# Optimization experiments

Hardware: AMD Instinct MI355X
Metric: run time of the kernel (lower is better)

## Reference

```python
import jax, jax.numpy as jnp
import numpy as np

B, K, N, T, C = 2, 2, 4096, 8, 3
H = 192            # hidden_dim
NODE_DIM = 10
N_LAYERS = 10
KNN = 16           # k nearest neighbours
TOP_FRAC = 0.4
SHARP = 5.0        # mask_sharpness
S = max(int(TOP_FRAC * N), KNN + 1)   # n_select per graph


def _ln(x, g, b, eps=1e-5):
    mu = x.mean(-1, keepdims=True)
    v = ((x - mu) ** 2).mean(-1, keepdims=True)  # biased var, matches nn.LayerNorm
    return (x - mu) / jnp.sqrt(v + eps) * g + b


def setup_inputs() -> dict:
    key = jax.random.key(0)
    ks = jax.random.split(key, 12)
    rn = lambda k, shape: 0.05 * jax.random.normal(k, shape, jnp.float32)
    F0 = 2 * NODE_DIM + 4   # first EdgeConv MLP in-dim
    FR = 2 * H + 4          # remaining EdgeConv MLP in-dim
    L = N_LAYERS - 1
    return {
        "u_base": jax.random.normal(ks[0], (B, K, N, C), jnp.float32),
        "pos": jax.random.uniform(ks[1], (B, N, 3), dtype=jnp.float32),
        "velocity_in": jax.random.normal(ks[2], (B, T, N, C), jnp.float32),
        "airfoil_mask": (jax.random.uniform(ks[3], (B, N)) < 0.05).astype(jnp.float32),
        "conv0_w1": rn(ks[4], (F0, H)), "conv0_b1": jnp.zeros((H,)),
        "conv0_w2": rn(ks[5], (H, H)), "conv0_b2": jnp.zeros((H,)),
        "conv0_g": jnp.ones((H,)), "conv0_be": jnp.zeros((H,)),
        "convs_w1": rn(ks[6], (L, FR, H)), "convs_b1": jnp.zeros((L, H)),
        "convs_w2": rn(ks[7], (L, H, H)), "convs_b2": jnp.zeros((L, H)),
        "convs_g": jnp.ones((L, H)), "convs_be": jnp.zeros((L, H)),
        "head_g": jnp.ones((H,)), "head_be": jnp.zeros((H,)),
        "head_w1": rn(ks[8], (H, H)), "head_b1": jnp.zeros((H,)),
        "head_w2": rn(ks[9], (H, 3)), "head_b2": jnp.zeros((3,)),
    }


def reference(u_base, pos, velocity_in, airfoil_mask,
              conv0_w1, conv0_b1, conv0_w2, conv0_b2, conv0_g, conv0_be,
              convs_w1, convs_b1, convs_w2, convs_b2, convs_g, convs_be,
              head_g, head_be, head_w1, head_b1, head_w2, head_b2):
    # --- variance gating (torch .var/.std are unbiased) ---
    var_pp = jnp.var(velocity_in, axis=1, ddof=1).sum(-1)                      # [B,N]
    var_z = (var_pp - var_pp.mean(1, keepdims=True)) / (
        jnp.std(var_pp, axis=1, ddof=1, keepdims=True) + 1e-8)
    soft_mask = jax.nn.sigmoid(SHARP * var_z) * (1.0 - airfoil_mask)           # [B,N]

    # --- select top-variance points per graph ---
    _, top_idx = jax.lax.top_k(var_pp, S)                                      # [B,S]
    pos_sel = jnp.take_along_axis(pos, top_idx[..., None], axis=1)             # [B,S,3]
    mask_sel = jnp.take_along_axis(soft_mask, top_idx, axis=1)[..., None]      # [B,S,1]
    v_last = velocity_in[:, -1]                                                # [B,N,C]
    ub_sel = jnp.take_along_axis(u_base, top_idx[:, None, :, None], axis=2)    # [B,K,S,C]
    vl_sel = jnp.take_along_axis(v_last, top_idx[..., None], axis=1)           # [B,S,C]
    vf_sel = jnp.take_along_axis(var_pp[..., None], top_idx[..., None], axis=1)
    static = jnp.concatenate([vl_sel, pos_sel, vf_sel], -1)                    # [B,S,7]
    x0 = jnp.concatenate(
        [ub_sel, jnp.broadcast_to(static[:, None], (B, K, S, 7))], -1)         # [B,K,S,10]

    def per_graph(x, pos_b):  # x: [K,S,F0], pos_b: [S,3]
        # kNN graph (self excluded via +inf diagonal, as in the chunked cdist)
        d2 = jnp.sum((pos_b[:, None] - pos_b[None]) ** 2, -1)                  # [S,S]
        d2 = d2.at[jnp.arange(S), jnp.arange(S)].set(jnp.inf)
        _, knn = jax.lax.top_k(-d2, KNN)                                       # [S,KNN]
        # PyG convention with edge_index=stack([targets, sources]):
        # i = edge_index[1] = knn neighbours, j = edge_index[0] = centre nodes
        idx_i = knn.reshape(-1)                     # [E] aggregation targets
        idx_j = jnp.repeat(jnp.arange(S), KNN)      # [E]
        rel = pos_b[idx_i] - pos_b[idx_j]           # pos[edge_index[1]] - pos[edge_index[0]]
        dist = jnp.linalg.norm(rel, axis=-1, keepdims=True)
        ea = jnp.concatenate([rel, dist], -1)       # [E,4]
        ea_b = jnp.broadcast_to(ea, (K,) + ea.shape)

        def conv(h, w1, b1, w2, b2, g, be):
            hi = h[:, idx_i]
            hj = h[:, idx_j]
            m = jnp.concatenate([hi, hj - hi, ea_b], -1)                       # [K,E,2F+4]
            m = jax.nn.gelu(m @ w1 + b1, approximate=False) @ w2 + b2          # [K,E,H]
            agg = jnp.zeros((K, S, H), h.dtype).at[:, idx_i].add(m)
            return _ln(agg, g, be)

        h = conv(x, conv0_w1, conv0_b1, conv0_w2, conv0_b2, conv0_g, conv0_be)
        for l in range(N_LAYERS - 1):
            h = conv(h, convs_w1[l], convs_b1[l], convs_w2[l], convs_b2[l],
                     convs_g[l], convs_be[l]) + h
        hh = _ln(h, head_g, head_be)
        return jax.nn.gelu(hh @ head_w1 + head_b1, approximate=False) @ head_w2 + head_b2

    delta = jax.vmap(per_graph)(x0, pos_sel)        # [B,K,S,3]
    delta = delta * mask_sel[:, None]               # [B,1,S,1]

    def scatter_b(idx, d):  # idx [S], d [K,S,3]
        return jnp.zeros((K, N, C), d.dtype).at[:, idx].set(d)

    delta_full = jax.vmap(scatter_b)(top_idx, delta)            # [B,K,N,C]
    return (u_base + delta_full) * (1.0 - airfoil_mask)[:, None, :, None]
```

## Files before the change

kernel.cpp:

```cpp
#include <hip/hip_runtime.h>
#include <hip/hip_bf16.h>
#include <math.h>

#define B_ 2
#define K_ 2
#define NN_ 4096
#define T_ 8
#define C_ 3
#define H_ 192
#define S_ 1638
#define KK_ 16
#define E_ (S_*KK_)
#define NROW (B_*K_*S_)
#define SHARP_ 5.0f

typedef __hip_bfloat16 bf;
typedef unsigned long long ull;
typedef __bf16 bf16x8 __attribute__((ext_vector_type(8)));
typedef float f32x4 __attribute__((ext_vector_type(4)));

__device__ int   g_isbf16;
__device__ int   g_viol;
__device__ __align__(16) float g_var[B_*NN_];
__device__ __align__(16) float g_soft[B_*NN_];
__device__ __align__(16) float g_accum[B_*2];
__device__ __align__(16) int   g_topidx[B_*S_];
__device__ __align__(16) float g_possel[B_*S_*3];
__device__ __align__(16) float g_masksel[B_*S_];
__device__ __align__(16) float g_x0[NROW*10];
__device__ __align__(16) int   g_knn[B_*E_];
__device__ __align__(16) float g_ea[B_*E_*4];
__device__ __align__(16) int   g_indeg[B_*S_];
__device__ __align__(16) int   g_cursor[B_*S_];
__device__ __align__(16) int   g_off[B_*(S_+1)];
__device__ __align__(16) int   g_list[B_*E_];
__device__ __align__(16) float g_P[(size_t)NROW*H_];
__device__ __align__(16) bf    g_Qbf[(size_t)NROW*H_];
__device__ __align__(16) float g_h[(size_t)NROW*H_];
__device__ __align__(16) bf    g_hbf[(size_t)NROW*H_];
__device__ __align__(16) bf    g_abf[(size_t)NROW*H_];
__device__ __align__(16) bf    g_hh[(size_t)NROW*H_];
__device__ __align__(16) bf    g_t[(size_t)NROW*H_];
__device__ __align__(16) bf    g_w2p[(size_t)11*H_*H_];
__device__ __align__(16) bf    g_wcp[(size_t)9*H_*384];

__device__ __forceinline__ float bf2f(bf x){ return __bfloat162float(x); }
__device__ __forceinline__ float LD(const void* p, long i){
  return g_isbf16 ? __bfloat162float(((const bf*)p)[i]) : ((const float*)p)[i];
}
__device__ __forceinline__ float gelu_f(float x){ return 0.5f*x*(1.0f + erff(x*0.70710678118654752f)); }
__device__ __forceinline__ ull shfl_xor_u64(ull v, int m){
  unsigned lo = (unsigned)v, hi = (unsigned)(v >> 32);
  lo = __shfl_xor(lo, m, 64); hi = __shfl_xor(hi, m, 64);
  return ((ull)hi << 32) | lo;
}

__global__ void k_viol(const void* a, const void* b, const void* c){
  int t = threadIdx.x;
  const bf* pa = (const bf*)a; const bf* pb = (const bf*)b; const bf* pc = (const bf*)c;
  int bad = 0;
  #pragma unroll
  for (int s = 0; s < 2; ++s){
    float va = __bfloat162float(pa[t + s*256]);
    float vb = __bfloat162float(pb[t + s*256]);
    float vc = __bfloat162float(pc[t + s*256]);
    if (!(fabsf(va) <= 1000.f)) bad = 1;
    if (!(fabsf(vb) <= 1000.f)) bad = 1;
    if (!(fabsf(vc) <= 1000.f)) bad = 1;
  }
  if (threadIdx.x == 0) g_viol = 0;
  __syncthreads();
  if (bad) atomicOr(&g_viol, 1);
  __syncthreads();
  if (threadIdx.x == 0) g_isbf16 = (g_viol == 0) ? 1 : 0;
}

__global__ void k_zero(){
  int tid = blockIdx.x*256 + threadIdx.x;
  if (tid < B_*S_){ g_indeg[tid]=0; g_cursor[tid]=0; }
  if (tid < B_*2) g_accum[tid]=0.f;
}

__global__ void k_var(const void* __restrict__ vel){
  int b = blockIdx.y;
  int n = blockIdx.x*256 + threadIdx.x;
  float v = 0.f;
  #pragma unroll
  for (int c = 0; c < 3; ++c){
    float x[8];
    #pragma unroll
    for (int t = 0; t < 8; ++t)
      x[t] = LD(vel, ((long)(b*T_+t)*NN_ + n)*3 + c);
    float m = __fadd_rn(__fadd_rn(__fadd_rn(x[0],x[1]), __fadd_rn(x[2],x[3])),
                        __fadd_rn(__fadd_rn(x[4],x[5]), __fadd_rn(x[6],x[7]))) / 8.0f;
    float d[8];
    #pragma unroll
    for (int t = 0; t < 8; ++t){ float dd = __fadd_rn(x[t], -m); d[t] = __fmul_rn(dd,dd); }
    float sv = __fadd_rn(__fadd_rn(__fadd_rn(d[0],d[1]), __fadd_rn(d[2],d[3])),
                         __fadd_rn(__fadd_rn(d[4],d[5]), __fadd_rn(d[6],d[7])));
    v = __fadd_rn(v, sv / 7.0f);
  }
  g_var[b*NN_ + n] = v;
  float s1 = v, s2 = v*v;
  #pragma unroll
  for (int o = 32; o; o >>= 1){ s1 += __shfl_xor(s1,o,64); s2 += __shfl_xor(s2,o,64); }
  __shared__ float r1[4], r2[4];
  int lane = threadIdx.x & 63, wid = threadIdx.x >> 6;
  if (!lane){ r1[wid]=s1; r2[wid]=s2; }
  __syncthreads();
  if (threadIdx.x == 0){
    atomicAdd(&g_accum[b*2+0], r1[0]+r1[1]+r1[2]+r1[3]);
    atomicAdd(&g_accum[b*2+1], r2[0]+r2[1]+r2[2]+r2[3]);
  }
}

__global__ void k_soft(const void* __restrict__ air){
  int b = blockIdx.y;
  int n = blockIdx.x*256 + threadIdx.x;
  float S1 = g_accum[b*2], S2 = g_accum[b*2+1];
  float mean = S1*(1.f/NN_);
  float sd = sqrtf(fmaxf((S2 - S1*S1*(1.f/NN_))*(1.f/(NN_-1)), 0.f));
  float v = g_var[b*NN_+n];
  float z = (v-mean)/(sd+1e-8f);
  float sig = 1.f/(1.f+expf(-SHARP_*z));
  g_soft[b*NN_+n] = sig*(1.f - LD(air, b*NN_+n));
}

__global__ __launch_bounds__(256) void k_rank(){
  int b = blockIdx.y;
  int i = blockIdx.x*4 + (threadIdx.x >> 6);
  int lane = threadIdx.x & 63;
  float vi = g_var[b*NN_+i];
  int rank = 0;
  for (int j = lane; j < NN_; j += 64){
    float vj = g_var[b*NN_+j];
    rank += ((vj > vi) || (vj == vi && j < i)) ? 1 : 0;
  }
  #pragma unroll
  for (int o = 32; o; o >>= 1) rank += __shfl_xor(rank, o, 64);
  if (lane == 0 && rank < S_) g_topidx[b*S_ + rank] = i;
}

__global__ void k_gather(const void* __restrict__ pos, const void* __restrict__ ub,
                         const void* __restrict__ vel){
  int gi = blockIdx.x*256 + threadIdx.x;
  if (gi >= B_*S_) return;
  int b = gi / S_, s = gi - b*S_;
  int node = g_topidx[gi];
  float px = LD(pos, ((long)b*NN_+node)*3+0);
  float py = LD(pos, ((long)b*NN_+node)*3+1);
  float pz = LD(pos, ((long)b*NN_+node)*3+2);
  g_possel[gi*3+0]=px; g_possel[gi*3+1]=py; g_possel[gi*3+2]=pz;
  g_masksel[gi] = g_soft[b*NN_+node];
  float vf = g_var[b*NN_+node];
  float vl0 = LD(vel, ((long)(b*T_+7)*NN_+node)*3+0);
  float vl1 = LD(vel, ((long)(b*T_+7)*NN_+node)*3+1);
  float vl2 = LD(vel, ((long)(b*T_+7)*NN_+node)*3+2);
  for (int k = 0; k < K_; ++k){
    long row = (long)(b*K_+k)*S_ + s;
    float* x = g_x0 + row*10;
    x[0]=LD(ub, ((long)(b*K_+k)*NN_+node)*3+0);
    x[1]=LD(ub, ((long)(b*K_+k)*NN_+node)*3+1);
    x[2]=LD(ub, ((long)(b*K_+k)*NN_+node)*3+2);
    x[3]=vl0; x[4]=vl1; x[5]=vl2;
    x[6]=px;  x[7]=py;  x[8]=pz;
    x[9]=vf;
  }
}

__global__ __launch_bounds__(256) void k_knn(){
  __shared__ float px[S_], py[S_], pz[S_];
  int b = blockIdx.y;
  int j = blockIdx.x*4 + (threadIdx.x >> 6);
  int lane = threadIdx.x & 63;
  for (int t = threadIdx.x; t < S_; t += 256){
    px[t] = g_possel[(b*S_+t)*3+0];
    py[t] = g_possel[(b*S_+t)*3+1];
    pz[t] = g_possel[(b*S_+t)*3+2];
  }
  __syncthreads();
  if (j >= S_) return;
  float xj=px[j], yj=py[j], zj=pz[j];
  float dist[KK_]; int id[KK_];
  #pragma unroll
  for (int t = 0; t < KK_; ++t){ dist[t]=3.0e38f; id[t]=0x7fffffff; }
  for (int c = lane; c < S_; c += 64){
    if (c == j) continue;
    float dx=__fadd_rn(px[c],-xj), dy=__fadd_rn(py[c],-yj), dz=__fadd_rn(pz[c],-zj);
    float d2 = __fadd_rn(__fadd_rn(__fmul_rn(dx,dx), __fmul_rn(dy,dy)), __fmul_rn(dz,dz));
    if (d2 < dist[KK_-1]){
      int p = 0;
      #pragma unroll
      for (int q = 0; q < KK_; ++q) p += (dist[q] <= d2) ? 1 : 0;
      #pragma unroll
      for (int q = KK_-1; q >= 1; --q){
        bool mv = (q > p);
        dist[q] = mv ? dist[q-1] : dist[q];
        id[q]   = mv ? id[q-1]   : id[q];
      }
      #pragma unroll
      for (int q = 0; q < KK_; ++q){ if (q == p){ dist[q] = d2; id[q] = c; } }
    }
  }
  ull mykey = 0;
  #pragma unroll
  for (int t = 0; t < KK_; ++t){
    ull k = (((ull)__float_as_uint(dist[0])) << 32) | (unsigned)id[0];
    ull m = k;
    #pragma unroll
    for (int o = 32; o; o >>= 1){ ull other = shfl_xor_u64(m, o); m = (other < m) ? other : m; }
    if (k == m){
      #pragma unroll
      for (int q = 0; q < KK_-1; ++q){ dist[q]=dist[q+1]; id[q]=id[q+1]; }
      dist[KK_-1] = 3.0e38f; id[KK_-1] = 0x7fffffff;
    }
    if (lane == t) mykey = m;
  }
  if (lane < KK_){
    int i = (int)(mykey & 0xffffffffu);
    g_knn[(b*S_+j)*KK_ + lane] = i;
    float rx = __fadd_rn(px[i],-xj), ry = __fadd_rn(py[i],-yj), rz = __fadd_rn(pz[i],-zj);
    float dd = sqrtf(__fadd_rn(__fadd_rn(__fmul_rn(rx,rx), __fmul_rn(ry,ry)), __fmul_rn(rz,rz)));
    float* o = g_ea + ((long)b*E_ + j*KK_ + lane)*4;
    o[0]=rx; o[1]=ry; o[2]=rz; o[3]=dd;
    atomicAdd(&g_indeg[b*S_+i], 1);
  }
}

__global__ void k_scan(){
  __shared__ int sA[2048], sB[2048];
  int b = blockIdx.x, tid = threadIdx.x;
  for (int i = tid; i < 2048; i += 1024) sA[i] = (i < S_) ? g_indeg[b*S_+i] : 0;
  __syncthreads();
  int *src = sA, *dst = sB;
  for (int d = 1; d < 2048; d <<= 1){
    for (int i = tid; i < 2048; i += 1024) dst[i] = src[i] + (i >= d ? src[i-d] : 0);
    __syncthreads();
    int* t2 = src; src = dst; dst = t2;
  }
  if (tid == 0) g_off[b*(S_+1)] = 0;
  for (int i = tid; i < S_; i += 1024) g_off[b*(S_+1)+i+1] = src[i];
}

__global__ void k_fill(){
  int idx = blockIdx.x*256 + threadIdx.x;
  if (idx >= B_*E_) return;
  int b = idx / E_, e = idx - b*E_;
  int i = g_knn[idx];
  int slot = atomicAdd(&g_cursor[b*S_+i], 1);
  g_list[b*E_ + g_off[b*(S_+1)+i] + slot] = e;
}

__global__ void k_pack_w2(const void* __restrict__ c0w2, const void* __restrict__ cw2,
                          const void* __restrict__ hw1){
  int gi = blockIdx.x*256 + threadIdx.x;
  if (gi >= 11*H_*H_) return;
  int mat = gi / (H_*H_), r = gi - mat*(H_*H_);
  int k = r / H_, n = r - (r/H_)*H_;
  float v;
  if (mat == 0)      v = LD(c0w2, (long)k*H_ + n);
  else if (mat <= 9) v = LD(cw2, (long)(mat-1)*H_*H_ + (long)k*H_ + n);
  else               v = LD(hw1, (long)k*H_ + n);
  int t = k>>5, q = (k>>3)&3, jj = k&7;
  g_w2p[(size_t)mat*H_*H_ + (((t*4+q)*H_ + n)*8 + jj)] = __float2bfloat16(v);
}

__global__ void k_pack_wc(const void* __restrict__ cw1){
  int gi = blockIdx.x*256 + threadIdx.x;
  if (gi >= 9*H_*384) return;
  int l = gi / (H_*384), r = gi - l*(H_*384);
  int k = r / 384, n = r - (r/384)*384;
  long base = (long)l*388*H_;
  float v;
  if (n < H_) v = LD(cw1, base + (long)k*H_ + n) - LD(cw1, base + (long)(H_+k)*H_ + n);
  else        v = LD(cw1, base + (long)(H_+k)*H_ + (n-H_));
  int t = k>>5, q = (k>>3)&3, jj = k&7;
  g_wcp[(size_t)l*(H_*384) + (((t*4+q)*384 + n)*8 + jj)] = __float2bfloat16(v);
}

__global__ void k_proj0(const void* __restrict__ w1){
  int gi = blockIdx.x*256 + threadIdx.x;
  if (gi >= NROW*384) return;
  int row = gi / 384, n = gi - (gi/384)*384;
  const float* x = g_x0 + (size_t)row*10;
  float acc = 0.f;
  if (n < H_){
    #pragma unroll
    for (int f = 0; f < 10; ++f) acc += x[f] * (LD(w1, f*H_+n) - LD(w1, (10+f)*H_+n));
    g_P[(size_t)row*H_ + n] = acc;
  } else {
    int hc = n - H_;
    #pragma unroll
    for (int f = 0; f < 10; ++f) acc += x[f] * LD(w1, (10+f)*H_+hc);
    g_Qbf[(size_t)row*H_ + hc] = __float2bfloat16(acc);
  }
}

__global__ __launch_bounds__(256) void k_gemmPQ(int bOff, int M){
  const bf* A  = g_hbf;
  const bf* Bp = g_wcp + bOff;
  int wave = threadIdx.x >> 6, lane = threadIdx.x & 63;
  int q = lane >> 4, l16 = lane & 15;
  long rowBase = (long)blockIdx.x * 32;
  f32x4 acc[2][6];
  #pragma unroll
  for (int rt = 0; rt < 2; ++rt)
    #pragma unroll
    for (int ct = 0; ct < 6; ++ct) acc[rt][ct] = (f32x4){0.f,0.f,0.f,0.f};
  #pragma unroll
  for (int t = 0; t < 6; ++t){
    int kof = t*32 + q*8;
    bf16x8 af[2], bfr[6];
    #pragma unroll
    for (int rt = 0; rt < 2; ++rt){
      long r = rowBase + rt*16 + l16;
      if (r >= M) r = M-1;
      af[rt] = *reinterpret_cast<const bf16x8*>(A + r*192 + kof);
    }
    #pragma unroll
    for (int ct = 0; ct < 6; ++ct){
      int n = wave*96 + ct*16 + l16;
      bfr[ct] = *reinterpret_cast<const bf16x8*>(Bp + (((t*4+q)*384 + n)*8));
    }
    #pragma unroll
    for (int rt = 0; rt < 2; ++rt)
      #pragma unroll
      for (int ct = 0; ct < 6; ++ct)
        acc[rt][ct] = __builtin_amdgcn_mfma_f32_16x16x32_bf16(af[rt], bfr[ct], acc[rt][ct], 0,0,0);
  }
  #pragma unroll
  for (int rt = 0; rt < 2; ++rt){
    #pragma unroll
    for (int ct = 0; ct < 6; ++ct){
      int col = wave*96 + ct*16 + l16;
      #pragma unroll
      for (int r = 0; r < 4; ++r){
        long row = rowBase + rt*16 + q*4 + r;
        if (row < M){
          float v = acc[rt][ct][r];
          if (col < 192) g_P[row*192 + col] = v;
          else           g_Qbf[row*192 + (col-192)] = __float2bfloat16(v);
        }
      }
    }
  }
}

template<int RES>
__global__ __launch_bounds__(256) void k_gemmln(const void* __restrict__ biasB, long biasO,
                                                const void* __restrict__ gB, long gO,
                                                const void* __restrict__ beB, long beO,
                                                int bOff, int M){
  const bf* A  = g_abf;
  const bf* Bp = g_w2p + bOff;
  int wave = threadIdx.x >> 6, lane = threadIdx.x & 63;
  int q = lane >> 4, l16 = lane & 15;
  long rowBase = (long)blockIdx.x * 32;
  f32x4 acc[2][3];
  #pragma unroll
  for (int rt = 0; rt < 2; ++rt)
    #pragma unroll
    for (int ct = 0; ct < 3; ++ct) acc[rt][ct] = (f32x4){0.f,0.f,0.f,0.f};
  #pragma unroll
  for (int t = 0; t < 6; ++t){
    int kof = t*32 + q*8;
    bf16x8 af[2], bfr[3];
    #pragma unroll
    for (int rt = 0; rt < 2; ++rt){
      long r = rowBase + rt*16 + l16;
      if (r >= M) r = M-1;
      af[rt] = *reinterpret_cast<const bf16x8*>(A + r*192 + kof);
    }
    #pragma unroll
    for (int ct = 0; ct < 3; ++ct){
      int n = wave*48 + ct*16 + l16;
      bfr[ct] = *reinterpret_cast<const bf16x8*>(Bp + (((t*4+q)*192 + n)*8));
    }
    #pragma unroll
    for (int rt = 0; rt < 2; ++rt)
      #pragma unroll
      for (int ct = 0; ct < 3; ++ct)
        acc[rt][ct] = __builtin_amdgcn_mfma_f32_16x16x32_bf16(af[rt], bfr[ct], acc[rt][ct], 0,0,0);
  }
  __shared__ float tile[32][200];
  __shared__ float srow[32], rrow[32];
  #pragma unroll
  for (int rt = 0; rt < 2; ++rt){
    #pragma unroll
    for (int ct = 0; ct < 3; ++ct){
      int col = wave*48 + ct*16 + l16;
      float bb = LD(biasB, biasO + col);
      #pragma unroll
      for (int r = 0; r < 4; ++r){
        int lr = rt*16 + q*4 + r;
        long row = rowBase + lr;
        long rowc = (row < M) ? row : (M-1);
        int bk = (int)(rowc / S_); int i = (int)(rowc - (long)bk*S_); int b = bk >> 1;
        float degf = (float)(g_off[b*(S_+1)+i+1] - g_off[b*(S_+1)+i]);
        tile[lr][col] = acc[rt][ct][r] + degf*bb;
      }
    }
  }
  __syncthreads();
  {
    int lr = threadIdx.x >> 3;
    int k8 = threadIdx.x & 7;
    float s = 0.f, qq = 0.f;
    for (int c = k8; c < 192; c += 8){ float x = tile[lr][c]; s += x; qq += x*x; }
    #pragma unroll
    for (int o = 1; o < 8; o <<= 1){ s += __shfl_xor(s,o,64); qq += __shfl_xor(qq,o,64); }
    if (k8 == 0){
      float mu = s*(1.f/H_);
      float var = qq*(1.f/H_) - mu*mu;
      srow[lr] = mu;
      rrow[lr] = rsqrtf(fmaxf(var, 0.f) + 1e-5f);
    }
  }
  __syncthreads();
  #pragma unroll
  for (int rt = 0; rt < 2; ++rt){
    #pragma unroll
    for (int ct = 0; ct < 3; ++ct){
      int col = wave*48 + ct*16 + l16;
      float gg = LD(gB, gO+col), be = LD(beB, beO+col);
      #pragma unroll
      for (int r = 0; r < 4; ++r){
        int lr = rt*16 + q*4 + r;
        long row = rowBase + lr;
        if (row < M){
          float y = (tile[lr][col] - srow[lr])*rrow[lr]*gg + be;
          if (RES) y += g_h[row*192 + col];
          g_h[row*192 + col] = y;
          g_hbf[row*192 + col] = __float2bfloat16(y);
        }
      }
    }
  }
}

__global__ __launch_bounds__(256) void k_gemmhead(const void* __restrict__ biasB,
                                                  int bOff, int M){
  const bf* A  = g_hh;
  const bf* Bp = g_w2p + bOff;
  int wave = threadIdx.x >> 6, lane = threadIdx.x & 63;
  int q = lane >> 4, l16 = lane & 15;
  long rowBase = (long)blockIdx.x * 32;
  f32x4 acc[2][3];
  #pragma unroll
  for (int rt = 0; rt < 2; ++rt)
    #pragma unroll
    for (int ct = 0; ct < 3; ++ct) acc[rt][ct] = (f32x4){0.f,0.f,0.f,0.f};
  #pragma unroll
  for (int t = 0; t < 6; ++t){
    int kof = t*32 + q*8;
    bf16x8 af[2], bfr[3];
    #pragma unroll
    for (int rt = 0; rt < 2; ++rt){
      long r = rowBase + rt*16 + l16;
      if (r >= M) r = M-1;
      af[rt] = *reinterpret_cast<const bf16x8*>(A + r*192 + kof);
    }
    #pragma unroll
    for (int ct = 0; ct < 3; ++ct){
      int n = wave*48 + ct*16 + l16;
      bfr[ct] = *reinterpret_cast<const bf16x8*>(Bp + (((t*4+q)*192 + n)*8));
    }
    #pragma unroll
    for (int rt = 0; rt < 2; ++rt)
      #pragma unroll
      for (int ct = 0; ct < 3; ++ct)
        acc[rt][ct] = __builtin_amdgcn_mfma_f32_16x16x32_bf16(af[rt], bfr[ct], acc[rt][ct], 0,0,0);
  }
  #pragma unroll
  for (int rt = 0; rt < 2; ++rt){
    #pragma unroll
    for (int ct = 0; ct < 3; ++ct){
      int col = wave*48 + ct*16 + l16;
      float bb = LD(biasB, col);
      #pragma unroll
      for (int r = 0; r < 4; ++r){
        long row = rowBase + rt*16 + q*4 + r;
        if (row < M) g_t[row*192 + col] = __float2bfloat16(gelu_f(acc[rt][ct][r] + bb));
      }
    }
  }
}

__global__ __launch_bounds__(192) void k_aggedge(const void* __restrict__ w1cB, long w1cO,
                                                 const void* __restrict__ b1B, long b1O){
  int row = blockIdx.x;
  int col = threadIdx.x;
  int bk = row / S_, i = row - bk*S_, b = bk >> 1;
  int off = g_off[b*(S_+1)+i];
  int deg = g_off[b*(S_+1)+i+1] - off;
  float w0 = LD(w1cB, w1cO+col),       w1v = LD(w1cB, w1cO+H_+col);
  float w2v = LD(w1cB, w1cO+2*H_+col), w3v = LD(w1cB, w1cO+3*H_+col);
  float base = g_P[(size_t)row*H_ + col] + LD(b1B, b1O+col);
  const int* lst = g_list + b*E_ + off;
  const bf* Q = g_Qbf + (size_t)bk*S_*H_;
  const float* EA = g_ea + (size_t)b*E_*4;
  float acc = 0.f;
  int d = 0;
  for (; d + 4 <= deg; d += 4){
    int e0 = lst[d], e1 = lst[d+1], e2 = lst[d+2], e3 = lst[d+3];
    float4 a0 = *reinterpret_cast<const float4*>(EA + (size_t)e0*4);
    float4 a1 = *reinterpret_cast<const float4*>(EA + (size_t)e1*4);
    float4 a2 = *reinterpret_cast<const float4*>(EA + (size_t)e2*4);
    float4 a3 = *reinterpret_cast<const float4*>(EA + (size_t)e3*4);
    float q0 = bf2f(Q[(size_t)(e0>>4)*H_ + col]);
    float q1 = bf2f(Q[(size_t)(e1>>4)*H_ + col]);
    float q2 = bf2f(Q[(size_t)(e2>>4)*H_ + col]);
    float q3 = bf2f(Q[(size_t)(e3>>4)*H_ + col]);
    acc += gelu_f(base + q0 + a0.x*w0 + a0.y*w1v + a0.z*w2v + a0.w*w3v);
    acc += gelu_f(base + q1 + a1.x*w0 + a1.y*w1v + a1.z*w2v + a1.w*w3v);
    acc += gelu_f(base + q2 + a2.x*w0 + a2.y*w1v + a2.z*w2v + a2.w*w3v);
    acc += gelu_f(base + q3 + a3.x*w0 + a3.y*w1v + a3.z*w2v + a3.w*w3v);
  }
  for (; d < deg; ++d){
    int e = lst[d];
    float4 a = *reinterpret_cast<const float4*>(EA + (size_t)e*4);
    float qv = bf2f(Q[(size_t)(e>>4)*H_ + col]);
    acc += gelu_f(base + qv + a.x*w0 + a.y*w1v + a.z*w2v + a.w*w3v);
  }
  g_abf[(size_t)row*H_ + col] = __float2bfloat16(acc);
}

__global__ void k_lnhead(const void* __restrict__ g, const void* __restrict__ be){
  int row = blockIdx.x;
  int col = threadIdx.x;
  float x = g_h[(size_t)row*H_ + col];
  float s = x, qq = x*x;
  #pragma unroll
  for (int o = 32; o; o >>= 1){ s += __shfl_xor(s,o,64); qq += __shfl_xor(qq,o,64); }
  __shared__ float ws[3][2];
  int wid = col >> 6, lane = col & 63;
  if (!lane){ ws[wid][0]=s; ws[wid][1]=qq; }
  __syncthreads();
  float Sm = ws[0][0]+ws[1][0]+ws[2][0];
  float Qm = ws[0][1]+ws[1][1]+ws[2][1];
  float mu = Sm*(1.f/H_);
  float var = Qm*(1.f/H_) - mu*mu;
  float rstd = rsqrtf(fmaxf(var, 0.f) + 1e-5f);
  g_hh[(size_t)row*H_ + col] = __float2bfloat16((x-mu)*rstd*LD(g,col) + LD(be,col));
}

__global__ void k_initout(const void* __restrict__ ub, const void* __restrict__ air, float* __restrict__ out){
  int gi = blockIdx.x*256 + threadIdx.x;
  int n = (gi/3) % NN_;
  int b = gi / (K_*NN_*C_);
  float a = 1.f - LD(air, b*NN_+n);
  out[gi] = LD(ub, gi) * a;
}

__global__ void k_headout(const void* __restrict__ w2, const void* __restrict__ b2,
                          const void* __restrict__ ub, const void* __restrict__ air,
                          float* __restrict__ out){
  int row = blockIdx.x*4 + (threadIdx.x >> 6);
  int lane = threadIdx.x & 63;
  if (row >= NROW) return;
  float t0 = bf2f(g_t[(size_t)row*H_ + lane]);
  float t1 = bf2f(g_t[(size_t)row*H_ + lane + 64]);
  float t2 = bf2f(g_t[(size_t)row*H_ + lane + 128]);
  float d[3];
  #pragma unroll
  for (int c = 0; c < 3; ++c){
    float p = t0*LD(w2,lane*3+c) + t1*LD(w2,(lane+64)*3+c) + t2*LD(w2,(lane+128)*3+c);
    #pragma unroll
    for (int o = 32; o; o >>= 1) p += __shfl_xor(p,o,64);
    d[c] = p + LD(b2,c);
  }
  if (lane == 0){
    int bk = row / S_, s = row - bk*S_, b = bk >> 1;
    float msk = g_masksel[b*S_+s];
    int node = g_topidx[b*S_+s];
    float am = 1.f - LD(air, b*NN_+node);
    #pragma unroll
    for (int c = 0; c < 3; ++c){
      long oi = ((long)bk*NN_ + node)*3 + c;
      out[oi] = (LD(ub,oi) + d[c]*msk)*am;
    }
  }
}

extern "C" void kernel_launch(void* const* d_in, const int* in_sizes, int n_in,
                              void* d_out, int out_size, void* d_ws, size_t ws_size,
                              hipStream_t stream) {
  (void)in_sizes; (void)n_in; (void)d_ws; (void)ws_size; (void)out_size;
  const void* u_base = d_in[0];
  const void* pos    = d_in[1];
  const void* vel    = d_in[2];
  const void* air    = d_in[3];
  const void* c0w1   = d_in[4];
  const void* c0b1   = d_in[5];
  const void* c0w2   = d_in[6];
  const void* c0b2   = d_in[7];
  const void* c0g    = d_in[8];
  const void* c0be   = d_in[9];
  const void* cw1    = d_in[10];
  const void* cb1    = d_in[11];
  const void* cw2    = d_in[12];
  const void* cb2    = d_in[13];
  const void* cg     = d_in[14];
  const void* cbe    = d_in[15];
  const void* hg     = d_in[16];
  const void* hbe    = d_in[17];
  const void* hw1    = d_in[18];
  const void* hb1    = d_in[19];
  const void* hw2    = d_in[20];
  const void* hb2    = d_in[21];
  float* out = (float*)d_out;

  k_viol<<<1, 256, 0, stream>>>(u_base, pos, vel);
  k_zero<<<13, 256, 0, stream>>>();
  k_var<<<dim3(16, B_), 256, 0, stream>>>(vel);
  k_soft<<<dim3(16, B_), 256, 0, stream>>>(air);
  k_rank<<<dim3(NN_/4, B_), 256, 0, stream>>>();
  k_gather<<<13, 256, 0, stream>>>(pos, u_base, vel);
  k_knn<<<dim3((S_+3)/4, B_), 256, 0, stream>>>();
  k_scan<<<B_, 1024, 0, stream>>>();
  k_fill<<<205, 256, 0, stream>>>();
  k_pack_w2<<<1584, 256, 0, stream>>>(c0w2, cw2, hw1);
  k_pack_wc<<<2592, 256, 0, stream>>>(cw1);
  k_initout<<<192, 256, 0, stream>>>(u_base, air, out);
  k_proj0<<<9828, 256, 0, stream>>>(c0w1);

  const int GN = (NROW + 31) / 32;
  for (int l = 0; l < 10; ++l){
    if (l > 0) k_gemmPQ<<<GN, 256, 0, stream>>>((l-1)*H_*384, NROW);

    long w1cO = (l == 0) ? 20L*H_ : ((long)(l-1)*388 + 384)*H_;
    const void* w1cB = (l == 0) ? c0w1 : cw1;
    long lOff = (l == 0) ? 0 : (long)(l-1)*H_;
    const void* b1B = (l == 0) ? c0b1 : cb1;
    k_aggedge<<<NROW, 192, 0, stream>>>(w1cB, w1cO, b1B, lOff);

    const void* b2B = (l == 0) ? c0b2 : cb2;
    const void* gB  = (l == 0) ? c0g  : cg;
    const void* beB = (l == 0) ? c0be : cbe;
    if (l > 0) k_gemmln<1><<<GN, 256, 0, stream>>>(b2B, lOff, gB, lOff, beB, lOff, l*H_*H_, NROW);
    else       k_gemmln<0><<<GN, 256, 0, stream>>>(b2B, lOff, gB, lOff, beB, lOff, l*H_*H_, NROW);
  }

  k_lnhead<<<NROW, 192, 0, stream>>>(hg, hbe);
  k_gemmhead<<<GN, 256, 0, stream>>>(hb1, 10*H_*H_, NROW);
  k_headout<<<NROW/4, 256, 0, stream>>>(hw2, hb2, u_base, air, out);
}
```

Measured before the change: 679.5 us.

## Fuse next-layer PQ projection into GEMM+LN epilogue and LN into head GEMM

Each layer's W2 GEMM + LayerNorm kernel now stages the normalized bf16 hidden state in shared memory and immediately runs the next layer's PQ projection GEMM from it. This removes the separate k_gemmPQ launch and the global g_hbf round trip. The head LayerNorm is folded into the head GEMM, and the soft-mask computation is moved into the gather kernel. k_viol/k_zero are merged and proj0 is tiled with weights cached in shared memory. The cost is higher shared memory and register use per block, which may lower occupancy.

```diff
diff --git a/kernel.cpp b/kernel.cpp
--- a/kernel.cpp
+++ b/kernel.cpp
@@ -22,7 +22,6 @@
 __device__ int   g_isbf16;
 __device__ int   g_viol;
 __device__ __align__(16) float g_var[B_*NN_];
-__device__ __align__(16) float g_soft[B_*NN_];
 __device__ __align__(16) float g_accum[B_*2];
 __device__ __align__(16) int   g_topidx[B_*S_];
 __device__ __align__(16) float g_possel[B_*S_*3];
@@ -37,9 +36,7 @@
 __device__ __align__(16) float g_P[(size_t)NROW*H_];
 __device__ __align__(16) bf    g_Qbf[(size_t)NROW*H_];
 __device__ __align__(16) float g_h[(size_t)NROW*H_];
-__device__ __align__(16) bf    g_hbf[(size_t)NROW*H_];
 __device__ __align__(16) bf    g_abf[(size_t)NROW*H_];
-__device__ __align__(16) bf    g_hh[(size_t)NROW*H_];
 __device__ __align__(16) bf    g_t[(size_t)NROW*H_];
 __device__ __align__(16) bf    g_w2p[(size_t)11*H_*H_];
 __device__ __align__(16) bf    g_wcp[(size_t)9*H_*384];
@@ -55,30 +52,29 @@
   return ((ull)hi << 32) | lo;
 }
 
-__global__ void k_viol(const void* a, const void* b, const void* c){
-  int t = threadIdx.x;
-  const bf* pa = (const bf*)a; const bf* pb = (const bf*)b; const bf* pc = (const bf*)c;
-  int bad = 0;
-  #pragma unroll
-  for (int s = 0; s < 2; ++s){
-    float va = __bfloat162float(pa[t + s*256]);
-    float vb = __bfloat162float(pb[t + s*256]);
-    float vc = __bfloat162float(pc[t + s*256]);
-    if (!(fabsf(va) <= 1000.f)) bad = 1;
-    if (!(fabsf(vb) <= 1000.f)) bad = 1;
-    if (!(fabsf(vc) <= 1000.f)) bad = 1;
-  }
-  if (threadIdx.x == 0) g_viol = 0;
-  __syncthreads();
-  if (bad) atomicOr(&g_viol, 1);
-  __syncthreads();
-  if (threadIdx.x == 0) g_isbf16 = (g_viol == 0) ? 1 : 0;
-}
-
-__global__ void k_zero(){
+__global__ void k_vz(const void* a, const void* b, const void* c){
   int tid = blockIdx.x*256 + threadIdx.x;
   if (tid < B_*S_){ g_indeg[tid]=0; g_cursor[tid]=0; }
   if (tid < B_*2) g_accum[tid]=0.f;
+  if (blockIdx.x == 0){
+    int t = threadIdx.x;
+    const bf* pa = (const bf*)a; const bf* pb = (const bf*)b; const bf* pc = (const bf*)c;
+    int bad = 0;
+    #pragma unroll
+    for (int s = 0; s < 2; ++s){
+      float va = __bfloat162float(pa[t + s*256]);
+      float vb = __bfloat162float(pb[t + s*256]);
+      float vc = __bfloat162float(pc[t + s*256]);
+      if (!(fabsf(va) <= 1000.f)) bad = 1;
+      if (!(fabsf(vb) <= 1000.f)) bad = 1;
+      if (!(fabsf(vc) <= 1000.f)) bad = 1;
+    }
+    if (threadIdx.x == 0) g_viol = 0;
+    __syncthreads();
+    if (bad) atomicOr(&g_viol, 1);
+    __syncthreads();
+    if (threadIdx.x == 0) g_isbf16 = (g_viol == 0) ? 1 : 0;
+  }
 }
 
 __global__ void k_var(const void* __restrict__ vel){
@@ -112,18 +108,6 @@
     atomicAdd(&g_accum[b*2+0], r1[0]+r1[1]+r1[2]+r1[3]);
     atomicAdd(&g_accum[b*2+1], r2[0]+r2[1]+r2[2]+r2[3]);
   }
-}
-
-__global__ void k_soft(const void* __restrict__ air){
-  int b = blockIdx.y;
-  int n = blockIdx.x*256 + threadIdx.x;
-  float S1 = g_accum[b*2], S2 = g_accum[b*2+1];
-  float mean = S1*(1.f/NN_);
-  float sd = sqrtf(fmaxf((S2 - S1*S1*(1.f/NN_))*(1.f/(NN_-1)), 0.f));
-  float v = g_var[b*NN_+n];
-  float z = (v-mean)/(sd+1e-8f);
-  float sig = 1.f/(1.f+expf(-SHARP_*z));
-  g_soft[b*NN_+n] = sig*(1.f - LD(air, b*NN_+n));
 }
 
 __global__ __launch_bounds__(256) void k_rank(){
@@ -142,7 +126,7 @@
 }
 
 __global__ void k_gather(const void* __restrict__ pos, const void* __restrict__ ub,
-                         const void* __restrict__ vel){
+                         const void* __restrict__ vel, const void* __restrict__ air){
   int gi = blockIdx.x*256 + threadIdx.x;
   if (gi >= B_*S_) return;
   int b = gi / S_, s = gi - b*S_;
@@ -151,8 +135,13 @@
   float py = LD(pos, ((long)b*NN_+node)*3+1);
   float pz = LD(pos, ((long)b*NN_+node)*3+2);
   g_possel[gi*3+0]=px; g_possel[gi*3+1]=py; g_possel[gi*3+2]=pz;
-  g_masksel[gi] = g_soft[b*NN_+node];
+  float S1 = g_accum[b*2], S2 = g_accum[b*2+1];
+  float mean = S1*(1.f/NN_);
+  float sd = sqrtf(fmaxf((S2 - S1*S1*(1.f/NN_))*(1.f/(NN_-1)), 0.f));
   float vf = g_var[b*NN_+node];
+  float z = (vf-mean)/(sd+1e-8f);
+  float sig = 1.f/(1.f+expf(-SHARP_*z));
+  g_masksel[gi] = sig*(1.f - LD(air, b*NN_+node));
   float vl0 = LD(vel, ((long)(b*T_+7)*NN_+node)*3+0);
   float vl1 = LD(vel, ((long)(b*T_+7)*NN_+node)*3+1);
   float vl2 = LD(vel, ((long)(b*T_+7)*NN_+node)*3+2);
@@ -278,210 +267,37 @@
   g_wcp[(size_t)l*(H_*384) + (((t*4+q)*384 + n)*8 + jj)] = __float2bfloat16(v);
 }
 
-__global__ void k_proj0(const void* __restrict__ w1){
-  int gi = blockIdx.x*256 + threadIdx.x;
-  if (gi >= NROW*384) return;
-  int row = gi / 384, n = gi - (gi/384)*384;
-  const float* x = g_x0 + (size_t)row*10;
-  float acc = 0.f;
-  if (n < H_){
-    #pragma unroll
-    for (int f = 0; f < 10; ++f) acc += x[f] * (LD(w1, f*H_+n) - LD(w1, (10+f)*H_+n));
-    g_P[(size_t)row*H_ + n] = acc;
-  } else {
-    int hc = n - H_;
-    #pragma unroll
-    for (int f = 0; f < 10; ++f) acc += x[f] * LD(w1, (10+f)*H_+hc);
-    g_Qbf[(size_t)row*H_ + hc] = __float2bfloat16(acc);
-  }
-}
-
-__global__ __launch_bounds__(256) void k_gemmPQ(int bOff, int M){
-  const bf* A  = g_hbf;
-  const bf* Bp = g_wcp + bOff;
-  int wave = threadIdx.x >> 6, lane = threadIdx.x & 63;
-  int q = lane >> 4, l16 = lane & 15;
-  long rowBase = (long)blockIdx.x * 32;
-  f32x4 acc[2][6];
-  #pragma unroll
-  for (int rt = 0; rt < 2; ++rt)
-    #pragma unroll
-    for (int ct = 0; ct < 6; ++ct) acc[rt][ct] = (f32x4){0.f,0.f,0.f,0.f};
-  #pragma unroll
-  for (int t = 0; t < 6; ++t){
-    int kof = t*32 + q*8;
-    bf16x8 af[2], bfr[6];
-    #pragma unroll
-    for (int rt = 0; rt < 2; ++rt){
-      long r = rowBase + rt*16 + l16;
-      if (r >= M) r = M-1;
-      af[rt] = *reinterpret_cast<const bf16x8*>(A + r*192 + kof);
-    }
-    #pragma unroll
-    for (int ct = 0; ct < 6; ++ct){
-      int n = wave*96 + ct*16 + l16;
-      bfr[ct] = *reinterpret_cast<const bf16x8*>(Bp + (((t*4+q)*384 + n)*8));
-    }
-    #pragma unroll
-    for (int rt = 0; rt < 2; ++rt)
-      #pragma unroll
-      for (int ct = 0; ct < 6; ++ct)
-        acc[rt][ct] = __builtin_amdgcn_mfma_f32_16x16x32_bf16(af[rt], bfr[ct], acc[rt][ct], 0,0,0);
-  }
-  #pragma unroll
-  for (int rt = 0; rt < 2; ++rt){
-    #pragma unroll
-    for (int ct = 0; ct < 6; ++ct){
-      int col = wave*96 + ct*16 + l16;
-      #pragma unroll
-      for (int r = 0; r < 4; ++r){
-        long row = rowBase + rt*16 + q*4 + r;
-        if (row < M){
-          float v = acc[rt][ct][r];
-          if (col < 192) g_P[row*192 + col] = v;
-          else           g_Qbf[row*192 + (col-192)] = __float2bfloat16(v);
-        }
-      }
-    }
-  }
-}
-
-template<int RES>
-__global__ __launch_bounds__(256) void k_gemmln(const void* __restrict__ biasB, long biasO,
-                                                const void* __restrict__ gB, long gO,
-                                                const void* __restrict__ beB, long beO,
-                                                int bOff, int M){
-  const bf* A  = g_abf;
-  const bf* Bp = g_w2p + bOff;
-  int wave = threadIdx.x >> 6, lane = threadIdx.x & 63;
-  int q = lane >> 4, l16 = lane & 15;
-  long rowBase = (long)blockIdx.x * 32;
-  f32x4 acc[2][3];
-  #pragma unroll
-  for (int rt = 0; rt < 2; ++rt)
-    #pragma unroll
-    for (int ct = 0; ct < 3; ++ct) acc[rt][ct] = (f32x4){0.f,0.f,0.f,0.f};
-  #pragma unroll
-  for (int t = 0; t < 6; ++t){
-    int kof = t*32 + q*8;
-    bf16x8 af[2], bfr[3];
-    #pragma unroll
-    for (int rt = 0; rt < 2; ++rt){
-      long r = rowBase + rt*16 + l16;
-      if (r >= M) r = M-1;
-      af[rt] = *reinterpret_cast<const bf16x8*>(A + r*192 + kof);
-    }
-    #pragma unroll
-    for (int ct = 0; ct < 3; ++ct){
-      int n = wave*48 + ct*16 + l16;
-      bfr[ct] = *reinterpret_cast<const bf16x8*>(Bp + (((t*4+q)*192 + n)*8));
-    }
-    #pragma unroll
-    for (int rt = 0; rt < 2; ++rt)
-      #pragma unroll
-      for (int ct = 0; ct < 3; ++ct)
-        acc[rt][ct] = __builtin_amdgcn_mfma_f32_16x16x32_bf16(af[rt], bfr[ct], acc[rt][ct], 0,0,0);
-  }
-  __shared__ float tile[32][200];
-  __shared__ float srow[32], rrow[32];
-  #pragma unroll
-  for (int rt = 0; rt < 2; ++rt){
-    #pragma unroll
-    for (int ct = 0; ct < 3; ++ct){
-      int col = wave*48 + ct*16 + l16;
-      float bb = LD(biasB, biasO + col);
-      #pragma unroll
-      for (int r = 0; r < 4; ++r){
-        int lr = rt*16 + q*4 + r;
-        long row = rowBase + lr;
-        long rowc = (row < M) ? row : (M-1);
-        int bk = (int)(rowc / S_); int i = (int)(rowc - (long)bk*S_); int b = bk >> 1;
-        float degf = (float)(g_off[b*(S_+1)+i+1] - g_off[b*(S_+1)+i]);
-        tile[lr][col] = acc[rt][ct][r] + degf*bb;
-      }
-    }
-  }
-  __syncthreads();
-  {
-    int lr = threadIdx.x >> 3;
-    int k8 = threadIdx.x & 7;
-    float s = 0.f, qq = 0.f;
-    for (int c = k8; c < 192; c += 8){ float x = tile[lr][c]; s += x; qq += x*x; }
-    #pragma unroll
-    for (int o = 1; o < 8; o <<= 1){ s += __shfl_xor(s,o,64); qq += __shfl_xor(qq,o,64); }
-    if (k8 == 0){
-      float mu = s*(1.f/H_);
-      float var = qq*(1.f/H_) - mu*mu;
-      srow[lr] = mu;
-      rrow[lr] = rsqrtf(fmaxf(var, 0.f) + 1e-5f);
-    }
-  }
-  __syncthreads();
-  #pragma unroll
-  for (int rt = 0; rt < 2; ++rt){
-    #pragma unroll
-    for (int ct = 0; ct < 3; ++ct){
-      int col = wave*48 + ct*16 + l16;
-      float gg = LD(gB, gO+col), be = LD(beB, beO+col);
-      #pragma unroll
-      for (int r = 0; r < 4; ++r){
-        int lr = rt*16 + q*4 + r;
-        long row = rowBase + lr;
-        if (row < M){
-          float y = (tile[lr][col] - srow[lr])*rrow[lr]*gg + be;
-          if (RES) y += g_h[row*192 + col];
-          g_h[row*192 + col] = y;
-          g_hbf[row*192 + col] = __float2bfloat16(y);
-        }
-      }
-    }
-  }
-}
-
-__global__ __launch_bounds__(256) void k_gemmhead(const void* __restrict__ biasB,
-                                                  int bOff, int M){
-  const bf* A  = g_hh;
-  const bf* Bp = g_w2p + bOff;
-  int wave = threadIdx.x >> 6, lane = threadIdx.x & 63;
-  int q = lane >> 4, l16 = lane & 15;
-  long rowBase = (long)blockIdx.x * 32;
-  f32x4 acc[2][3];
-  #pragma unroll
-  for (int rt = 0; rt < 2; ++rt)
-    #pragma unroll
-    for (int ct = 0; ct < 3; ++ct) acc[rt][ct] = (f32x4){0.f,0.f,0.f,0.f};
-  #pragma unroll
-  for (int t = 0; t < 6; ++t){
-    int kof = t*32 + q*8;
-    bf16x8 af[2], bfr[3];
-    #pragma unroll
-    for (int rt = 0; rt < 2; ++rt){
-      long r = rowBase + rt*16 + l16;
-      if (r >= M) r = M-1;
-      af[rt] = *reinterpret_cast<const bf16x8*>(A + r*192 + kof);
-    }
-    #pragma unroll
-    for (int ct = 0; ct < 3; ++ct){
-      int n = wave*48 + ct*16 + l16;
-      bfr[ct] = *reinterpret_cast<const bf16x8*>(Bp + (((t*4+q)*192 + n)*8));
-    }
-    #pragma unroll
-    for (int rt = 0; rt < 2; ++rt)
-      #pragma unroll
-      for (int ct = 0; ct < 3; ++ct)
-        acc[rt][ct] = __builtin_amdgcn_mfma_f32_16x16x32_bf16(af[rt], bfr[ct], acc[rt][ct], 0,0,0);
-  }
-  #pragma unroll
-  for (int rt = 0; rt < 2; ++rt){
-    #pragma unroll
-    for (int ct = 0; ct < 3; ++ct){
-      int col = wave*48 + ct*16 + l16;
-      float bb = LD(biasB, col);
-      #pragma unroll
-      for (int r = 0; r < 4; ++r){
-        long row = rowBase + rt*16 + q*4 + r;
-        if (row < M) g_t[row*192 + col] = __float2bfloat16(gelu_f(acc[rt][ct][r] + bb));
-      }
+__global__ __launch_bounds__(256) void k_proj0(const void* __restrict__ w1){
+  __shared__ float xs[16][10];
+  __shared__ float wP[10][192];
+  __shared__ float wQ[10][192];
+  int tid = threadIdx.x;
+  long rowBase = (long)blockIdx.x * 16;
+  for (int idx = tid; idx < 1920; idx += 256){
+    int f = idx / 192, n = idx - (idx/192)*192;
+    float a = LD(w1, f*H_+n), b = LD(w1, (10+f)*H_+n);
+    wP[f][n] = a - b; wQ[f][n] = b;
+  }
+  for (int idx = tid; idx < 160; idx += 256){
+    int r = idx / 10, f = idx - (idx/10)*10;
+    long row = rowBase + r; if (row >= NROW) row = NROW-1;
+    xs[r][f] = g_x0[row*10 + f];
+  }
+  __syncthreads();
+  for (int o = tid; o < 16*384; o += 256){
+    int r = o / 384, n = o - (o/384)*384;
+    long row = rowBase + r;
+    if (row >= NROW) continue;
+    float acc = 0.f;
+    if (n < 192){
+      #pragma unroll
+      for (int f = 0; f < 10; ++f) acc += xs[r][f]*wP[f][n];
+      g_P[row*192 + n] = acc;
+    } else {
+      int nc = n - 192;
+      #pragma unroll
+      for (int f = 0; f < 10; ++f) acc += xs[r][f]*wQ[f][nc];
+      g_Qbf[row*192 + nc] = __float2bfloat16(acc);
     }
   }
 }
@@ -525,23 +341,204 @@
   g_abf[(size_t)row*H_ + col] = __float2bfloat16(acc);
 }
 
-__global__ void k_lnhead(const void* __restrict__ g, const void* __restrict__ be){
-  int row = blockIdx.x;
-  int col = threadIdx.x;
-  float x = g_h[(size_t)row*H_ + col];
-  float s = x, qq = x*x;
-  #pragma unroll
-  for (int o = 32; o; o >>= 1){ s += __shfl_xor(s,o,64); qq += __shfl_xor(qq,o,64); }
-  __shared__ float ws[3][2];
-  int wid = col >> 6, lane = col & 63;
-  if (!lane){ ws[wid][0]=s; ws[wid][1]=qq; }
-  __syncthreads();
-  float Sm = ws[0][0]+ws[1][0]+ws[2][0];
-  float Qm = ws[0][1]+ws[1][1]+ws[2][1];
-  float mu = Sm*(1.f/H_);
-  float var = Qm*(1.f/H_) - mu*mu;
-  float rstd = rsqrtf(fmaxf(var, 0.f) + 1e-5f);
-  g_hh[(size_t)row*H_ + col] = __float2bfloat16((x-mu)*rstd*LD(g,col) + LD(be,col));
+template<int RES, int DOPQ>
+__global__ __launch_bounds__(256) void k_gemmlnPQ(const void* __restrict__ biasB, long biasO,
+                                                  const void* __restrict__ gB, long gO,
+                                                  const void* __restrict__ beB, long beO,
+                                                  int bOff, int pqOff, int M){
+  const bf* Bp = g_w2p + bOff;
+  int wave = threadIdx.x >> 6, lane = threadIdx.x & 63;
+  int q = lane >> 4, l16 = lane & 15;
+  long rowBase = (long)blockIdx.x * 32;
+  f32x4 acc[2][3];
+  #pragma unroll
+  for (int rt = 0; rt < 2; ++rt)
+    #pragma unroll
+    for (int ct = 0; ct < 3; ++ct) acc[rt][ct] = (f32x4){0.f,0.f,0.f,0.f};
+  #pragma unroll
+  for (int t = 0; t < 6; ++t){
+    int kof = t*32 + q*8;
+    bf16x8 af[2], bfr[3];
+    #pragma unroll
+    for (int rt = 0; rt < 2; ++rt){
+      long r = rowBase + rt*16 + l16;
+      if (r >= M) r = M-1;
+      af[rt] = *reinterpret_cast<const bf16x8*>(g_abf + r*192 + kof);
+    }
+    #pragma unroll
+    for (int ct = 0; ct < 3; ++ct){
+      int n = wave*48 + ct*16 + l16;
+      bfr[ct] = *reinterpret_cast<const bf16x8*>(Bp + (((t*4+q)*192 + n)*8));
+    }
+    #pragma unroll
+    for (int rt = 0; rt < 2; ++rt)
+      #pragma unroll
+      for (int ct = 0; ct < 3; ++ct)
+        acc[rt][ct] = __builtin_amdgcn_mfma_f32_16x16x32_bf16(af[rt], bfr[ct], acc[rt][ct], 0,0,0);
+  }
+  __shared__ float tile[32][200];
+  __shared__ bf hb_s[32][216];
+  __shared__ float srow[32], rrow[32];
+  #pragma unroll
+  for (int rt = 0; rt < 2; ++rt){
+    #pragma unroll
+    for (int ct = 0; ct < 3; ++ct){
+      int col = wave*48 + ct*16 + l16;
+      float bb = LD(biasB, biasO + col);
+      #pragma unroll
+      for (int r = 0; r < 4; ++r){
+        int lr = rt*16 + q*4 + r;
+        long row = rowBase + lr;
+        long rowc = (row < M) ? row : (M-1);
+        int bk = (int)(rowc / S_); int i = (int)(rowc - (long)bk*S_); int b = bk >> 1;
+        float degf = (float)(g_off[b*(S_+1)+i+1] - g_off[b*(S_+1)+i]);
+        tile[lr][col] = acc[rt][ct][r] + degf*bb;
+      }
+    }
+  }
+  __syncthreads();
+  {
+    int lr = threadIdx.x >> 3;
+    int k8 = threadIdx.x & 7;
+    float s = 0.f, qq = 0.f;
+    for (int c = k8; c < 192; c += 8){ float x = tile[lr][c]; s += x; qq += x*x; }
+    #pragma unroll
+    for (int o = 1; o < 8; o <<= 1){ s += __shfl_xor(s,o,64); qq += __shfl_xor(qq,o,64); }
+    if (k8 == 0){
+      float mu = s*(1.f/H_);
+      float var = qq*(1.f/H_) - mu*mu;
+      srow[lr] = mu;
+      rrow[lr] = rsqrtf(fmaxf(var, 0.f) + 1e-5f);
+    }
+  }
+  __syncthreads();
+  for (int o = threadIdx.x; o < 32*192; o += 256){
+    int lr = o / 192, col = o - (o/192)*192;
+    long row = rowBase + lr;
+    float y = (tile[lr][col] - srow[lr])*rrow[lr]*LD(gB,gO+col) + LD(beB,beO+col);
+    if (RES && row < M) y += g_h[row*192 + col];
+    if (row < M) g_h[row*192 + col] = y;
+    hb_s[lr][col] = __float2bfloat16(y);
+  }
+  __syncthreads();
+  if constexpr (DOPQ){
+    const bf* Wp = g_wcp + pqOff;
+    f32x4 acc2[2][6];
+    #pragma unroll
+    for (int rt = 0; rt < 2; ++rt)
+      #pragma unroll
+      for (int ct = 0; ct < 6; ++ct) acc2[rt][ct] = (f32x4){0.f,0.f,0.f,0.f};
+    #pragma unroll
+    for (int t = 0; t < 6; ++t){
+      int kof = t*32 + q*8;
+      bf16x8 af[2], bfr[6];
+      #pragma unroll
+      for (int rt = 0; rt < 2; ++rt)
+        af[rt] = *reinterpret_cast<const bf16x8*>(&hb_s[rt*16 + l16][kof]);
+      #pragma unroll
+      for (int ct = 0; ct < 6; ++ct){
+        int n = wave*96 + ct*16 + l16;
+        bfr[ct] = *reinterpret_cast<const bf16x8*>(Wp + (((t*4+q)*384 + n)*8));
+      }
+      #pragma unroll
+      for (int rt = 0; rt < 2; ++rt)
+        #pragma unroll
+        for (int ct = 0; ct < 6; ++ct)
+          acc2[rt][ct] = __builtin_amdgcn_mfma_f32_16x16x32_bf16(af[rt], bfr[ct], acc2[rt][ct], 0,0,0);
+    }
+    #pragma unroll
+    for (int rt = 0; rt < 2; ++rt){
+      #pragma unroll
+      for (int ct = 0; ct < 6; ++ct){
+        int col = wave*96 + ct*16 + l16;
+        #pragma unroll
+        for (int r = 0; r < 4; ++r){
+          long row = rowBase + rt*16 + q*4 + r;
+          if (row < M){
+            float v = acc2[rt][ct][r];
+            if (col < 192) g_P[row*192 + col] = v;
+            else           g_Qbf[row*192 + (col-192)] = __float2bfloat16(v);
+          }
+        }
+      }
+    }
+  }
+}
+
+__global__ __launch_bounds__(256) void k_gemmhead(const void* __restrict__ gB,
+                                                  const void* __restrict__ beB,
+                                                  const void* __restrict__ biasB,
+                                                  int bOff, int M){
+  const bf* Bp = g_w2p + bOff;
+  int wave = threadIdx.x >> 6, lane = threadIdx.x & 63;
+  int q = lane >> 4, l16 = lane & 15;
+  long rowBase = (long)blockIdx.x * 32;
+  __shared__ float tile[32][200];
+  __shared__ bf hb_s[32][216];
+  __shared__ float srow[32], rrow[32];
+  for (int o = threadIdx.x; o < 32*192; o += 256){
+    int lr = o / 192, col = o - (o/192)*192;
+    long row = rowBase + lr;
+    long rowc = (row < M) ? row : (M-1);
+    tile[lr][col] = g_h[rowc*192 + col];
+  }
+  __syncthreads();
+  {
+    int lr = threadIdx.x >> 3;
+    int k8 = threadIdx.x & 7;
+    float s = 0.f, qq = 0.f;
+    for (int c = k8; c < 192; c += 8){ float x = tile[lr][c]; s += x; qq += x*x; }
+    #pragma unroll
+    for (int o = 1; o < 8; o <<= 1){ s += __shfl_xor(s,o,64); qq += __shfl_xor(qq,o,64); }
+    if (k8 == 0){
+      float mu = s*(1.f/H_);
+      float var = qq*(1.f/H_) - mu*mu;
+      srow[lr] = mu;
+      rrow[lr] = rsqrtf(fmaxf(var, 0.f) + 1e-5f);
+    }
+  }
+  __syncthreads();
+  for (int o = threadIdx.x; o < 32*192; o += 256){
+    int lr = o / 192, col = o - (o/192)*192;
+    hb_s[lr][col] = __float2bfloat16((tile[lr][col] - srow[lr])*rrow[lr]*LD(gB,col) + LD(beB,col));
+  }
+  __syncthreads();
+  f32x4 acc[2][3];
+  #pragma unroll
+  for (int rt = 0; rt < 2; ++rt)
+    #pragma unroll
+    for (int ct = 0; ct < 3; ++ct) acc[rt][ct] = (f32x4){0.f,0.f,0.f,0.f};
+  #pragma unroll
+  for (int t = 0; t < 6; ++t){
+    int kof = t*32 + q*8;
+    bf16x8 af[2], bfr[3];
+    #pragma unroll
+    for (int rt = 0; rt < 2; ++rt)
+      af[rt] = *reinterpret_cast<const bf16x8*>(&hb_s[rt*16 + l16][kof]);
+    #pragma unroll
+    for (int ct = 0; ct < 3; ++ct){
+      int n = wave*48 + ct*16 + l16;
+      bfr[ct] = *reinterpret_cast<const bf16x8*>(Bp + (((t*4+q)*192 + n)*8));
+    }
+    #pragma unroll
+    for (int rt = 0; rt < 2; ++rt)
+      #pragma unroll
+      for (int ct = 0; ct < 3; ++ct)
+        acc[rt][ct] = __builtin_amdgcn_mfma_f32_16x16x32_bf16(af[rt], bfr[ct], acc[rt][ct], 0,0,0);
+  }
+  #pragma unroll
+  for (int rt = 0; rt < 2; ++rt){
+    #pragma unroll
+    for (int ct = 0; ct < 3; ++ct){
+      int col = wave*48 + ct*16 + l16;
+      float bb = LD(biasB, col);
+      #pragma unroll
+      for (int r = 0; r < 4; ++r){
+        long row = rowBase + rt*16 + q*4 + r;
+        if (row < M) g_t[row*192 + col] = __float2bfloat16(gelu_f(acc[rt][ct][r] + bb));
+      }
+    }
+  }
 }
 
 __global__ void k_initout(const void* __restrict__ ub, const void* __restrict__ air, float* __restrict__ out){
@@ -610,24 +607,20 @@
   const void* hb2    = d_in[21];
   float* out = (float*)d_out;
 
-  k_viol<<<1, 256, 0, stream>>>(u_base, pos, vel);
-  k_zero<<<13, 256, 0, stream>>>();
+  k_vz<<<13, 256, 0, stream>>>(u_base, pos, vel);
   k_var<<<dim3(16, B_), 256, 0, stream>>>(vel);
-  k_soft<<<dim3(16, B_), 256, 0, stream>>>(air);
   k_rank<<<dim3(NN_/4, B_), 256, 0, stream>>>();
-  k_gather<<<13, 256, 0, stream>>>(pos, u_base, vel);
+  k_gather<<<13, 256, 0, stream>>>(pos, u_base, vel, air);
   k_knn<<<dim3((S_+3)/4, B_), 256, 0, stream>>>();
   k_scan<<<B_, 1024, 0, stream>>>();
   k_fill<<<205, 256, 0, stream>>>();
   k_pack_w2<<<1584, 256, 0, stream>>>(c0w2, cw2, hw1);
   k_pack_wc<<<2592, 256, 0, stream>>>(cw1);
   k_initout<<<192, 256, 0, stream>>>(u_base, air, out);
-  k_proj0<<<9828, 256, 0, stream>>>(c0w1);
+  k_proj0<<<410, 256, 0, stream>>>(c0w1);
 
   const int GN = (NROW + 31) / 32;
   for (int l = 0; l < 10; ++l){
-    if (l > 0) k_gemmPQ<<<GN, 256, 0, stream>>>((l-1)*H_*384, NROW);
-
     long w1cO = (l == 0) ? 20L*H_ : ((long)(l-1)*388 + 384)*H_;
     const void* w1cB = (l == 0) ? c0w1 : cw1;
     long lOff = (l == 0) ? 0 : (long)(l-1)*H_;
@@ -637,11 +630,12 @@
     const void* b2B = (l == 0) ? c0b2 : cb2;
     const void* gB  = (l == 0) ? c0g  : cg;
     const void* beB = (l == 0) ? c0be : cbe;
-    if (l > 0) k_gemmln<1><<<GN, 256, 0, stream>>>(b2B, lOff, gB, lOff, beB, lOff, l*H_*H_, NROW);
-    else       k_gemmln<0><<<GN, 256, 0, stream>>>(b2B, lOff, gB, lOff, beB, lOff, l*H_*H_, NROW);
-  }
-
-  k_lnhead<<<NROW, 192, 0, stream>>>(hg, hbe);
-  k_gemmhead<<<GN, 256, 0, stream>>>(hb1, 10*H_*H_, NROW);
+    int pqOff = l*H_*384;
+    if (l == 0)      k_gemmlnPQ<0,1><<<GN, 256, 0, stream>>>(b2B, lOff, gB, lOff, beB, lOff, l*H_*H_, pqOff, NROW);
+    else if (l < 9)  k_gemmlnPQ<1,1><<<GN, 256, 0, stream>>>(b2B, lOff, gB, lOff, beB, lOff, l*H_*H_, pqOff, NROW);
+    else             k_gemmlnPQ<1,0><<<GN, 256, 0, stream>>>(b2B, lOff, gB, lOff, beB, lOff, l*H_*H_, 0, NROW);
+  }
+
+  k_gemmhead<<<GN, 256, 0, stream>>>(hg, hbe, hb1, 10*H_*H_, NROW);
   k_headout<<<NROW/4, 256, 0, stream>>>(hw2, hb2, u_base, air, out);
 }
```

New measurement: 704.4 us. +3.7%, slower.
